# Kernel tuning notes

Hardware: AMD Instinct MI355X
Metric: run time of the kernel (lower is better)

Reference implementation:

```python
import jax, jax.numpy as jnp
import numpy as np

N_NODES = 100000
N_EDGES = 1200000
IN_CH = 64
HID = 64
OUT_CH = 8
N_GRAPHS = 256


def setup_inputs() -> dict:
    key = jax.random.key(0)
    ks = jax.random.split(key, 12)
    x = jax.random.normal(ks[0], (N_NODES, IN_CH), dtype=jnp.float32)
    edge_index = jax.random.randint(ks[1], (2, N_EDGES), 0, N_NODES, dtype=jnp.int64)
    batch = jnp.sort(jax.random.randint(ks[2], (N_NODES,), 0, N_GRAPHS, dtype=jnp.int64))
    s1 = 1.0 / np.sqrt(IN_CH)
    s2 = 1.0 / np.sqrt(HID)
    # SAGEConv: lin_l (aggregated neighbors, with bias), lin_r (root, no bias)
    W1l = jax.random.uniform(ks[3], (HID, IN_CH), jnp.float32, -s1, s1)
    b1l = jax.random.uniform(ks[4], (HID,), jnp.float32, -s1, s1)
    W1r = jax.random.uniform(ks[5], (HID, IN_CH), jnp.float32, -s1, s1)
    W2l = jax.random.uniform(ks[6], (HID, HID), jnp.float32, -s2, s2)
    b2l = jax.random.uniform(ks[7], (HID,), jnp.float32, -s2, s2)
    W2r = jax.random.uniform(ks[8], (HID, HID), jnp.float32, -s2, s2)
    Wc = jax.random.uniform(ks[9], (OUT_CH, HID), jnp.float32, -s2, s2)
    bc = jax.random.uniform(ks[10], (OUT_CH,), jnp.float32, -s2, s2)
    return {"x": x, "edge_index": edge_index, "batch": batch,
            "W1l": W1l, "b1l": b1l, "W1r": W1r,
            "W2l": W2l, "b2l": b2l, "W2r": W2r,
            "Wc": Wc, "bc": bc}


def _sage_conv(x, src, dst, Wl, bl, Wr):
    # mean aggregation of neighbor (source) features onto targets
    agg = jax.ops.segment_sum(x[src], dst, num_segments=x.shape[0])  # [N, d]
    cnt = jax.ops.segment_sum(jnp.ones((src.shape[0],), x.dtype), dst,
                              num_segments=x.shape[0])
    agg = agg / jnp.maximum(cnt, 1.0)[:, None]
    return agg @ Wl.T + bl + x @ Wr.T


def reference(x, edge_index, batch, W1l, b1l, W1r, W2l, b2l, W2r, Wc, bc):
    src, dst = edge_index[0], edge_index[1]
    h = jax.nn.relu(_sage_conv(x, src, dst, W1l, b1l, W1r))
    # dropout p=0.2 is identity in eval mode
    h = jax.nn.relu(_sage_conv(h, src, dst, W2l, b2l, W2r))
    # global mean pool over graphs
    gsum = jax.ops.segment_sum(h, batch, num_segments=N_GRAPHS)      # [G, HID]
    gcnt = jax.ops.segment_sum(jnp.ones((h.shape[0],), h.dtype), batch,
                               num_segments=N_GRAPHS)
    g = gsum / jnp.maximum(gcnt, 1.0)[:, None]
    return g @ Wc.T + bc
```

## Files before the change

### kernel.cpp

```cpp
#include <hip/hip_runtime.h>

#define N_NODES 100000
#define N_EDGES 1200000
#define CH 64
#define NG 256
#define OC 8
#define NBUK 196
#define BINCHUNK 4096
#define NBLKA 293
#define NSTRIP 6250
#define ZERO_U4 4224

typedef unsigned short ushort_t;
typedef unsigned int uint_t;
typedef __attribute__((ext_vector_type(8))) short bf16x8;
typedef __attribute__((ext_vector_type(4))) float f32x4;

__device__ __forceinline__ ushort_t f2bf(float f) {
  uint_t u = __float_as_uint(f);
  return (ushort_t)((u + 0x7FFFu + ((u >> 16) & 1u)) >> 16);
}
__device__ __forceinline__ float bf2f(ushort_t b) {
  return __uint_as_float(((uint_t)b) << 16);
}

__global__ void prep_k(const float* __restrict__ W1l, const float* __restrict__ W1r,
                       const float* __restrict__ W2l, const float* __restrict__ W2r,
                       ushort_t* __restrict__ wb, uint4* __restrict__ zr) {
  const int gi = blockIdx.x * blockDim.x + threadIdx.x;
  for (int i = gi; i < ZERO_U4; i += gridDim.x * blockDim.x)
    zr[i] = make_uint4(0, 0, 0, 0);
  if (blockIdx.x == 0) {
    for (int k = threadIdx.x; k < CH * CH; k += 256) {
      wb[k]               = f2bf(W1l[k]);
      wb[k + CH * CH]     = f2bf(W1r[k]);
      wb[k + 2 * CH * CH] = f2bf(W2l[k]);
      wb[k + 3 * CH * CH] = f2bf(W2r[k]);
    }
  }
}

__global__ __launch_bounds__(256) void countA_k(const int* __restrict__ dst,
                                                int* __restrict__ gbase) {
  __shared__ int hist[NBUK];
  for (int i = threadIdx.x; i < NBUK; i += 256) hist[i] = 0;
  __syncthreads();
  const int cs = blockIdx.x * BINCHUNK;
  int ce = cs + BINCHUNK;
  if (ce > N_EDGES) ce = N_EDGES;
  for (int e = cs + threadIdx.x; e < ce; e += 256)
    atomicAdd(&hist[dst[e] >> 9], 1);
  __syncthreads();
  for (int b = threadIdx.x; b < NBUK; b += 256) {
    int c = hist[b];
    if (c) atomicAdd(&gbase[b], c);
  }
}

__global__ void scanB_k(const int* __restrict__ gbase, int* __restrict__ boff,
                        int* __restrict__ cursor) {
  __shared__ int s[256];
  int v = (threadIdx.x < NBUK) ? gbase[threadIdx.x] : 0;
  s[threadIdx.x] = v;
  __syncthreads();
  for (int o = 1; o < 256; o <<= 1) {
    int t = (threadIdx.x >= o) ? s[threadIdx.x - o] : 0;
    __syncthreads();
    s[threadIdx.x] += t;
    __syncthreads();
  }
  if (threadIdx.x < NBUK) {
    int ex = s[threadIdx.x] - v;
    boff[threadIdx.x] = ex;
    cursor[threadIdx.x] = ex;
  }
  if (threadIdx.x == NBUK - 1) boff[NBUK] = s[threadIdx.x];
}

__global__ __launch_bounds__(256) void scatterA_k(const int* __restrict__ src,
                                                  const int* __restrict__ dst,
                                                  int* __restrict__ cursor,
                                                  int* __restrict__ tmp) {
  __shared__ int hist[NBUK];
  for (int i = threadIdx.x; i < NBUK; i += 256) hist[i] = 0;
  __syncthreads();
  const int cs = blockIdx.x * BINCHUNK;
  int ce = cs + BINCHUNK;
  if (ce > N_EDGES) ce = N_EDGES;
  for (int e = cs + threadIdx.x; e < ce; e += 256)
    atomicAdd(&hist[dst[e] >> 9], 1);
  __syncthreads();
  for (int b = threadIdx.x; b < NBUK; b += 256) {
    int c = hist[b];
    hist[b] = c ? atomicAdd(&cursor[b], c) : 0;
  }
  __syncthreads();
  for (int e = cs + threadIdx.x; e < ce; e += 256) {
    int d = dst[e];
    int slot = atomicAdd(&hist[d >> 9], 1);
    tmp[slot] = (src[e] << 9) | (d & 511);
  }
}

__global__ __launch_bounds__(512) void csrC_k(const int* __restrict__ tmp,
                                              const int* __restrict__ boff,
                                              int* __restrict__ rp,
                                              int* __restrict__ col) {
  __shared__ int lh[512];
  __shared__ int s[512];
  const int b = blockIdx.x;
  const int tid = threadIdx.x;
  const int eb = boff[b], ee = boff[b + 1];
  lh[tid] = 0;
  __syncthreads();
  for (int e = eb + tid; e < ee; e += 512) atomicAdd(&lh[tmp[e] & 511], 1);
  __syncthreads();
  int v = lh[tid];
  s[tid] = v;
  __syncthreads();
  for (int o = 1; o < 512; o <<= 1) {
    int t = (tid >= o) ? s[tid - o] : 0;
    __syncthreads();
    s[tid] += t;
    __syncthreads();
  }
  const int base = eb + s[tid] - v;
  const int node = b * 512 + tid;
  if (node < N_NODES) rp[node] = base;
  if (b == 0 && tid == 0) rp[N_NODES] = N_EDGES;
  lh[tid] = base;
  __syncthreads();
  for (int e = eb + tid; e < ee; e += 512) {
    int p = tmp[e];
    int slot = atomicAdd(&lh[p & 511], 1);
    col[slot] = (p >> 9) * CH;
  }
}

template <typename TIN>
__global__ __launch_bounds__(256) void transform_mfma_k(
    const TIN* __restrict__ in, const ushort_t* __restrict__ Wlb,
    const ushort_t* __restrict__ Wrb, ushort_t* __restrict__ outl,
    ushort_t* __restrict__ outr) {
  const int wid = blockIdx.x * 4 + (threadIdx.x >> 6);
  if (wid >= NSTRIP) return;
  const int lane = threadIdx.x & 63;
  const int row = lane & 15;
  const int kb = lane >> 4;

  bf16x8 Bfrag[8][2];
#pragma unroll
  for (int t = 0; t < 8; ++t) {
    const ushort_t* W = (t < 4) ? Wlb : Wrb;
    const int j = (t & 3) * 16 + row;
#pragma unroll
    for (int h = 0; h < 2; ++h)
      Bfrag[t][h] = *(const bf16x8*)(W + j * CH + h * 32 + kb * 8);
  }

  const int n0 = wid * 16;
  bf16x8 Afrag[2];
#pragma unroll
  for (int h = 0; h < 2; ++h) {
    if constexpr (sizeof(TIN) == 4) {
      const float* p = (const float*)in + (size_t)(n0 + row) * CH + h * 32 + kb * 8;
      float4 a0 = *(const float4*)p;
      float4 a1 = *(const float4*)(p + 4);
      bf16x8 a;
      a[0] = (short)f2bf(a0.x); a[1] = (short)f2bf(a0.y);
      a[2] = (short)f2bf(a0.z); a[3] = (short)f2bf(a0.w);
      a[4] = (short)f2bf(a1.x); a[5] = (short)f2bf(a1.y);
      a[6] = (short)f2bf(a1.z); a[7] = (short)f2bf(a1.w);
      Afrag[h] = a;
    } else {
      const ushort_t* p =
          (const ushort_t*)in + (size_t)(n0 + row) * CH + h * 32 + kb * 8;
      Afrag[h] = *(const bf16x8*)p;
    }
  }

  f32x4 acc[8];
#pragma unroll
  for (int t = 0; t < 8; ++t) {
    acc[t] = (f32x4){0.f, 0.f, 0.f, 0.f};
    acc[t] = __builtin_amdgcn_mfma_f32_16x16x32_bf16(Afrag[0], Bfrag[t][0],
                                                     acc[t], 0, 0, 0);
    acc[t] = __builtin_amdgcn_mfma_f32_16x16x32_bf16(Afrag[1], Bfrag[t][1],
                                                     acc[t], 0, 0, 0);
  }

  const int orow = (lane >> 4) * 4;
#pragma unroll
  for (int t = 0; t < 4; ++t)
#pragma unroll
    for (int i = 0; i < 4; ++i)
      outl[(size_t)(n0 + orow + i) * CH + t * 16 + row] = f2bf(acc[t][i]);
#pragma unroll
  for (int t = 4; t < 8; ++t)
#pragma unroll
    for (int i = 0; i < 4; ++i)
      outr[(size_t)(n0 + orow + i) * CH + (t - 4) * 16 + row] = f2bf(acc[t][i]);
}

template <int MODE>
__global__ __launch_bounds__(256) void gather_k(
    const ushort_t* __restrict__ gl, const ushort_t* __restrict__ gr,
    const float* __restrict__ bl, const int* __restrict__ rowptr,
    const int* __restrict__ col, ushort_t* __restrict__ outh,
    const int* __restrict__ batch, float* __restrict__ gsum,
    int* __restrict__ gcnt) {
  const int lane = threadIdx.x & 63;
  const float biasv = bl[lane];
  const int wid = blockIdx.x * (blockDim.x >> 6) + (threadIdx.x >> 6);
  const int nw = gridDim.x * (blockDim.x >> 6);
  const int per = (N_NODES + nw - 1) / nw;
  int ns = wid * per;
  int ne = ns + per;
  if (ne > N_NODES) ne = N_NODES;
  if (ns >= ne) return;

  int curg = -1;
  float paccv = 0.f;
  int pcnt = 0;

  for (int n = ns; n < ne; ++n) {
    const int eb = rowptr[n], ee = rowptr[n + 1];
    float a0 = 0.f, a1 = 0.f, a2 = 0.f, a3 = 0.f;
    float a4 = 0.f, a5 = 0.f, a6 = 0.f, a7 = 0.f;
    int i = eb;
    for (; i + 8 <= ee; i += 8) {
      int c0 = col[i],     c1 = col[i + 1], c2 = col[i + 2], c3 = col[i + 3];
      int c4 = col[i + 4], c5 = col[i + 5], c6 = col[i + 6], c7 = col[i + 7];
      a0 += bf2f(gl[(size_t)c0 + lane]);
      a1 += bf2f(gl[(size_t)c1 + lane]);
      a2 += bf2f(gl[(size_t)c2 + lane]);
      a3 += bf2f(gl[(size_t)c3 + lane]);
      a4 += bf2f(gl[(size_t)c4 + lane]);
      a5 += bf2f(gl[(size_t)c5 + lane]);
      a6 += bf2f(gl[(size_t)c6 + lane]);
      a7 += bf2f(gl[(size_t)c7 + lane]);
    }
    for (; i + 4 <= ee; i += 4) {
      int c0 = col[i], c1 = col[i + 1], c2 = col[i + 2], c3 = col[i + 3];
      a0 += bf2f(gl[(size_t)c0 + lane]);
      a1 += bf2f(gl[(size_t)c1 + lane]);
      a2 += bf2f(gl[(size_t)c2 + lane]);
      a3 += bf2f(gl[(size_t)c3 + lane]);
    }
    for (; i < ee; ++i) a0 += bf2f(gl[(size_t)col[i] + lane]);
    const int deg = ee - eb;
    const float inv = deg > 0 ? 1.f / (float)deg : 1.f;
    const float s = ((a0 + a1) + (a2 + a3)) + ((a4 + a5) + (a6 + a7));
    const ushort_t gv = __builtin_nontemporal_load(&gr[(size_t)n * CH + lane]);
    const float r = fmaxf(fmaf(s, inv, biasv + bf2f(gv)), 0.f);
    if (MODE == 0) {
      __builtin_nontemporal_store(f2bf(r), &outh[(size_t)n * CH + lane]);
    } else {
      int g = batch[n];
      if (g != curg) {
        if (curg >= 0) {
          atomicAdd(&gsum[curg * CH + lane], paccv);
          if (lane == 0) atomicAdd(&gcnt[curg], pcnt);
        }
        curg = g;
        paccv = 0.f;
        pcnt = 0;
      }
      paccv += r;
      pcnt++;
    }
  }
  if (MODE == 1 && curg >= 0) {
    atomicAdd(&gsum[curg * CH + lane], paccv);
    if (lane == 0) atomicAdd(&gcnt[curg], pcnt);
  }
}

__global__ void final_k(const float* __restrict__ gsum, const int* __restrict__ gcnt,
                        const float* __restrict__ Wc, const float* __restrict__ bc,
                        float* __restrict__ out) {
  __shared__ float Wcs[OC * CH];
  __shared__ float bcs[OC];
  for (int i = threadIdx.x; i < OC * CH; i += blockDim.x) Wcs[i] = Wc[i];
  if (threadIdx.x < OC) bcs[threadIdx.x] = bc[threadIdx.x];
  __syncthreads();
  int g = threadIdx.x;
  float c = (float)gcnt[g];
  float inv = c > 0.f ? 1.f / c : 1.f;
  float gr[CH];
#pragma unroll
  for (int k = 0; k < CH; ++k) gr[k] = gsum[g * CH + k] * inv;
#pragma unroll
  for (int o = 0; o < OC; ++o) {
    float acc = bcs[o];
#pragma unroll
    for (int k = 0; k < CH; ++k) acc += gr[k] * Wcs[o * CH + k];
    out[g * OC + o] = acc;
  }
}

extern "C" void kernel_launch(void* const* d_in, const int* in_sizes, int n_in,
                              void* d_out, int out_size, void* d_ws, size_t ws_size,
                              hipStream_t stream) {
  const float* x   = (const float*)d_in[0];
  const int*   ei  = (const int*)d_in[1];
  const int*   bat = (const int*)d_in[2];
  const float* W1l = (const float*)d_in[3];
  const float* b1l = (const float*)d_in[4];
  const float* W1r = (const float*)d_in[5];
  const float* W2l = (const float*)d_in[6];
  const float* b2l = (const float*)d_in[7];
  const float* W2r = (const float*)d_in[8];
  const float* Wc  = (const float*)d_in[9];
  const float* bc  = (const float*)d_in[10];
  float* out = (float*)d_out;

  char* ws = (char*)d_ws;
  ushort_t* buf1 = (ushort_t*)(ws + 0);
  ushort_t* buf3 = (ushort_t*)(ws + 12800000);
  ushort_t* buf2 = (ushort_t*)(ws + 25600000);
  int*   tmp     = (int*)(ws + 0);
  int*   rp      = (int*)(ws + 51200000);
  int*   col     = (int*)(ws + 51600128);
  float* gsum    = (float*)(ws + 56400128);
  int*   gcnt    = (int*)(ws + 56465664);
  int*   gbase   = (int*)(ws + 56466688);
  int*   boff    = (int*)(ws + 56467712);
  int*   cursor  = (int*)(ws + 56468736);
  ushort_t* wbf  = (ushort_t*)(ws + 56469760);

  const int* src = ei;
  const int* dst = ei + N_EDGES;

  prep_k<<<32, 256, 0, stream>>>(W1l, W1r, W2l, W2r, wbf,
                                 (uint4*)(ws + 56400128));
  countA_k<<<NBLKA, 256, 0, stream>>>(dst, gbase);
  scanB_k<<<1, 256, 0, stream>>>(gbase, boff, cursor);
  scatterA_k<<<NBLKA, 256, 0, stream>>>(src, dst, cursor, tmp);
  csrC_k<<<NBUK, 512, 0, stream>>>(tmp, boff, rp, col);

  transform_mfma_k<float><<<(NSTRIP + 3) / 4, 256, 0, stream>>>(
      x, wbf, wbf + CH * CH, buf1, buf2);
  gather_k<0><<<2048, 256, 0, stream>>>(buf1, buf2, b1l, rp, col, buf3,
                                        nullptr, nullptr, nullptr);
  transform_mfma_k<ushort_t><<<(NSTRIP + 3) / 4, 256, 0, stream>>>(
      buf3, wbf + 2 * CH * CH, wbf + 3 * CH * CH, buf1, buf2);
  gather_k<1><<<2048, 256, 0, stream>>>(buf1, buf2, b2l, rp, col, nullptr,
                                        bat, gsum, gcnt);
  final_k<<<1, 256, 0, stream>>>(gsum, gcnt, Wc, bc, out);
}
```

Measured before the change: 203.7 us.

## Fuse layer-1 gather with layer-2 MFMA transform via LDS strip staging

Merges the first-layer neighbor gather and the second-layer dense transform into one kernel. Each wave gathers 16 nodes, writes their activations into a swizzled LDS tile, then runs the MFMA transform on that tile directly. This removes one kernel launch and the global write and read of the intermediate hidden activations. In exchange, the gather now uses a fixed 16-node strip per wave instead of a balanced grid-stride split, so the gather runs with a different occupancy and load balance.

After: 231.2 us. +13.5%, slower.

```diff
diff --git a/kernel.cpp b/kernel.cpp
--- a/kernel.cpp
+++ b/kernel.cpp
@@ -137,9 +137,8 @@
   }
 }
 
-template <typename TIN>
 __global__ __launch_bounds__(256) void transform_mfma_k(
-    const TIN* __restrict__ in, const ushort_t* __restrict__ Wlb,
+    const float* __restrict__ in, const ushort_t* __restrict__ Wlb,
     const ushort_t* __restrict__ Wrb, ushort_t* __restrict__ outl,
     ushort_t* __restrict__ outr) {
   const int wid = blockIdx.x * 4 + (threadIdx.x >> 6);
@@ -162,21 +161,15 @@
   bf16x8 Afrag[2];
 #pragma unroll
   for (int h = 0; h < 2; ++h) {
-    if constexpr (sizeof(TIN) == 4) {
-      const float* p = (const float*)in + (size_t)(n0 + row) * CH + h * 32 + kb * 8;
-      float4 a0 = *(const float4*)p;
-      float4 a1 = *(const float4*)(p + 4);
-      bf16x8 a;
-      a[0] = (short)f2bf(a0.x); a[1] = (short)f2bf(a0.y);
-      a[2] = (short)f2bf(a0.z); a[3] = (short)f2bf(a0.w);
-      a[4] = (short)f2bf(a1.x); a[5] = (short)f2bf(a1.y);
-      a[6] = (short)f2bf(a1.z); a[7] = (short)f2bf(a1.w);
-      Afrag[h] = a;
-    } else {
-      const ushort_t* p =
-          (const ushort_t*)in + (size_t)(n0 + row) * CH + h * 32 + kb * 8;
-      Afrag[h] = *(const bf16x8*)p;
-    }
+    const float* p = in + (size_t)(n0 + row) * CH + h * 32 + kb * 8;
+    float4 a0 = *(const float4*)p;
+    float4 a1 = *(const float4*)(p + 4);
+    bf16x8 a;
+    a[0] = (short)f2bf(a0.x); a[1] = (short)f2bf(a0.y);
+    a[2] = (short)f2bf(a0.z); a[3] = (short)f2bf(a0.w);
+    a[4] = (short)f2bf(a1.x); a[5] = (short)f2bf(a1.y);
+    a[6] = (short)f2bf(a1.z); a[7] = (short)f2bf(a1.w);
+    Afrag[h] = a;
   }
 
   f32x4 acc[8];
@@ -202,13 +195,101 @@
       outr[(size_t)(n0 + orow + i) * CH + (t - 4) * 16 + row] = f2bf(acc[t][i]);
 }
 
-template <int MODE>
-__global__ __launch_bounds__(256) void gather_k(
+__global__ __launch_bounds__(256) void gather_t2_k(
     const ushort_t* __restrict__ gl, const ushort_t* __restrict__ gr,
     const float* __restrict__ bl, const int* __restrict__ rowptr,
-    const int* __restrict__ col, ushort_t* __restrict__ outh,
-    const int* __restrict__ batch, float* __restrict__ gsum,
-    int* __restrict__ gcnt) {
+    const int* __restrict__ col, const ushort_t* __restrict__ W2lb,
+    const ushort_t* __restrict__ W2rb, ushort_t* __restrict__ outl,
+    ushort_t* __restrict__ outr) {
+  __shared__ ushort_t lds[4][16][64];
+  const int wv = threadIdx.x >> 6;
+  const int lane = threadIdx.x & 63;
+  const int strip = blockIdx.x * 4 + wv;
+  if (strip >= NSTRIP) return;
+  const float biasv = bl[lane];
+  const int n0 = strip * 16;
+  ushort_t(*L)[64] = lds[wv];
+  const int sg = lane >> 3;
+  const int sw = lane & 7;
+
+  for (int i = 0; i < 16; ++i) {
+    const int n = n0 + i;
+    const int eb = rowptr[n], ee = rowptr[n + 1];
+    float a0 = 0.f, a1 = 0.f, a2 = 0.f, a3 = 0.f;
+    float a4 = 0.f, a5 = 0.f, a6 = 0.f, a7 = 0.f;
+    int e = eb;
+    for (; e + 8 <= ee; e += 8) {
+      int c0 = col[e],     c1 = col[e + 1], c2 = col[e + 2], c3 = col[e + 3];
+      int c4 = col[e + 4], c5 = col[e + 5], c6 = col[e + 6], c7 = col[e + 7];
+      a0 += bf2f(gl[(size_t)c0 + lane]);
+      a1 += bf2f(gl[(size_t)c1 + lane]);
+      a2 += bf2f(gl[(size_t)c2 + lane]);
+      a3 += bf2f(gl[(size_t)c3 + lane]);
+      a4 += bf2f(gl[(size_t)c4 + lane]);
+      a5 += bf2f(gl[(size_t)c5 + lane]);
+      a6 += bf2f(gl[(size_t)c6 + lane]);
+      a7 += bf2f(gl[(size_t)c7 + lane]);
+    }
+    for (; e + 4 <= ee; e += 4) {
+      int c0 = col[e], c1 = col[e + 1], c2 = col[e + 2], c3 = col[e + 3];
+      a0 += bf2f(gl[(size_t)c0 + lane]);
+      a1 += bf2f(gl[(size_t)c1 + lane]);
+      a2 += bf2f(gl[(size_t)c2 + lane]);
+      a3 += bf2f(gl[(size_t)c3 + lane]);
+    }
+    for (; e < ee; ++e) a0 += bf2f(gl[(size_t)col[e] + lane]);
+    const int deg = ee - eb;
+    const float inv = deg > 0 ? 1.f / (float)deg : 1.f;
+    const float s = ((a0 + a1) + (a2 + a3)) + ((a4 + a5) + (a6 + a7));
+    const ushort_t gv = __builtin_nontemporal_load(&gr[(size_t)n * CH + lane]);
+    const float r = fmaxf(fmaf(s, inv, biasv + bf2f(gv)), 0.f);
+    L[i][((sg ^ (i & 7)) << 3) | sw] = f2bf(r);
+  }
+
+  const int row = lane & 15;
+  const int kb = lane >> 4;
+  bf16x8 Bfrag[8][2];
+#pragma unroll
+  for (int t = 0; t < 8; ++t) {
+    const ushort_t* W = (t < 4) ? W2lb : W2rb;
+    const int j = (t & 3) * 16 + row;
+#pragma unroll
+    for (int h = 0; h < 2; ++h)
+      Bfrag[t][h] = *(const bf16x8*)(W + j * CH + h * 32 + kb * 8);
+  }
+  bf16x8 Afrag[2];
+#pragma unroll
+  for (int h = 0; h < 2; ++h) {
+    const int pg = (kb + 4 * h) ^ (row & 7);
+    Afrag[h] = *(const bf16x8*)&L[row][pg << 3];
+  }
+  f32x4 acc[8];
+#pragma unroll
+  for (int t = 0; t < 8; ++t) {
+    acc[t] = (f32x4){0.f, 0.f, 0.f, 0.f};
+    acc[t] = __builtin_amdgcn_mfma_f32_16x16x32_bf16(Afrag[0], Bfrag[t][0],
+                                                     acc[t], 0, 0, 0);
+    acc[t] = __builtin_amdgcn_mfma_f32_16x16x32_bf16(Afrag[1], Bfrag[t][1],
+                                                     acc[t], 0, 0, 0);
+  }
+  const int orow = (lane >> 4) * 4;
+#pragma unroll
+  for (int t = 0; t < 4; ++t)
+#pragma unroll
+    for (int i = 0; i < 4; ++i)
+      outl[(size_t)(n0 + orow + i) * CH + t * 16 + row] = f2bf(acc[t][i]);
+#pragma unroll
+  for (int t = 4; t < 8; ++t)
+#pragma unroll
+    for (int i = 0; i < 4; ++i)
+      outr[(size_t)(n0 + orow + i) * CH + (t - 4) * 16 + row] = f2bf(acc[t][i]);
+}
+
+__global__ __launch_bounds__(256) void gather_pool_k(
+    const ushort_t* __restrict__ gl, const ushort_t* __restrict__ gr,
+    const float* __restrict__ bl, const int* __restrict__ rowptr,
+    const int* __restrict__ col, const int* __restrict__ batch,
+    float* __restrict__ gsum, int* __restrict__ gcnt) {
   const int lane = threadIdx.x & 63;
   const float biasv = bl[lane];
   const int wid = blockIdx.x * (blockDim.x >> 6) + (threadIdx.x >> 6);
@@ -253,24 +334,20 @@
     const float s = ((a0 + a1) + (a2 + a3)) + ((a4 + a5) + (a6 + a7));
     const ushort_t gv = __builtin_nontemporal_load(&gr[(size_t)n * CH + lane]);
     const float r = fmaxf(fmaf(s, inv, biasv + bf2f(gv)), 0.f);
-    if (MODE == 0) {
-      __builtin_nontemporal_store(f2bf(r), &outh[(size_t)n * CH + lane]);
-    } else {
-      int g = batch[n];
-      if (g != curg) {
-        if (curg >= 0) {
-          atomicAdd(&gsum[curg * CH + lane], paccv);
-          if (lane == 0) atomicAdd(&gcnt[curg], pcnt);
-        }
-        curg = g;
-        paccv = 0.f;
-        pcnt = 0;
+    int g = batch[n];
+    if (g != curg) {
+      if (curg >= 0) {
+        atomicAdd(&gsum[curg * CH + lane], paccv);
+        if (lane == 0) atomicAdd(&gcnt[curg], pcnt);
       }
-      paccv += r;
-      pcnt++;
-    }
-  }
-  if (MODE == 1 && curg >= 0) {
+      curg = g;
+      paccv = 0.f;
+      pcnt = 0;
+    }
+    paccv += r;
+    pcnt++;
+  }
+  if (curg >= 0) {
     atomicAdd(&gsum[curg * CH + lane], paccv);
     if (lane == 0) atomicAdd(&gcnt[curg], pcnt);
   }
@@ -319,6 +396,7 @@
   ushort_t* buf1 = (ushort_t*)(ws + 0);
   ushort_t* buf3 = (ushort_t*)(ws + 12800000);
   ushort_t* buf2 = (ushort_t*)(ws + 25600000);
+  ushort_t* buf4 = (ushort_t*)(ws + 38400000);
   int*   tmp     = (int*)(ws + 0);
   int*   rp      = (int*)(ws + 51200000);
   int*   col     = (int*)(ws + 51600128);
@@ -339,13 +417,12 @@
   scatterA_k<<<NBLKA, 256, 0, stream>>>(src, dst, cursor, tmp);
   csrC_k<<<NBUK, 512, 0, stream>>>(tmp, boff, rp, col);
 
-  transform_mfma_k<float><<<(NSTRIP + 3) / 4, 256, 0, stream>>>(
+  transform_mfma_k<<<(NSTRIP + 3) / 4, 256, 0, stream>>>(
       x, wbf, wbf + CH * CH, buf1, buf2);
-  gather_k<0><<<2048, 256, 0, stream>>>(buf1, buf2, b1l, rp, col, buf3,
-                                        nullptr, nullptr, nullptr);
-  transform_mfma_k<ushort_t><<<(NSTRIP + 3) / 4, 256, 0, stream>>>(
-      buf3, wbf + 2 * CH * CH, wbf + 3 * CH * CH, buf1, buf2);
-  gather_k<1><<<2048, 256, 0, stream>>>(buf1, buf2, b2l, rp, col, nullptr,
-                                        bat, gsum, gcnt);
+  gather_t2_k<<<(NSTRIP + 3) / 4, 256, 0, stream>>>(
+      buf1, buf2, b1l, rp, col, wbf + 2 * CH * CH, wbf + 3 * CH * CH,
+      buf3, buf4);
+  gather_pool_k<<<2048, 256, 0, stream>>>(buf3, buf4, b2l, rp, col,
+                                          bat, gsum, gcnt);
   final_k<<<1, 256, 0, stream>>>(gsum, gcnt, Wc, bc, out);
 }
```
